# Performance work log

Measured on AMD Instinct MI355X. Metric: run time of the kernel, lower is better.

## Reference

```python
import jax, jax.numpy as jnp
import numpy as np

H = 64      # LSTM hidden units
OUT = 10    # dense softmax classes


def setup_inputs() -> dict:
    key = jax.random.key(0)
    k0, k1, k2, k3 = jax.random.split(key, 4)
    B, T, D = 256, 1024, 128
    x = jax.random.normal(k0, (B, T, D), dtype=jnp.float32)
    # small weight scale keeps relu cell state stable over 1024 steps
    W = jax.random.normal(k1, (D, 4 * H), dtype=jnp.float32) * 0.05
    U = jax.random.normal(k2, (H, 4 * H), dtype=jnp.float32) * 0.05
    b = jnp.zeros((4 * H,), jnp.float32)
    Wd = jax.random.normal(k3, (H, OUT), dtype=jnp.float32) * 0.05
    bd = jnp.zeros((OUT,), jnp.float32)
    return {"x": x, "W": W, "U": U, "b": b, "Wd": Wd, "bd": bd}


def hard_sigmoid(z):
    # legacy Keras recurrent_activation default
    return jnp.clip(0.2 * z + 0.5, 0.0, 1.0)


def lstm_last_hidden(x, W, U, b):
    # x: [B,T,D] -> last hidden state [B,H]
    B = x.shape[0]
    xw = jnp.einsum('btd,dg->btg', x, W) + b  # [B,T,4H] input projection, computed once

    def step(carry, xt):
        h, c = carry
        z = xt + h @ U  # [B,4H]
        i = hard_sigmoid(z[:, :H])
        f = hard_sigmoid(z[:, H:2 * H])
        g = jax.nn.relu(z[:, 2 * H:3 * H])   # activation='relu' (candidate)
        o = hard_sigmoid(z[:, 3 * H:])
        c = f * c + i * g
        h = o * jax.nn.relu(c)               # activation='relu' on cell output
        return (h, c), None

    h0 = jnp.zeros((B, H), x.dtype)
    (h, _), _ = jax.lax.scan(step, (h0, h0), jnp.swapaxes(xw, 0, 1))
    return h


def reference(x, W, U, b, Wd, bd):
    h = lstm_last_hidden(x, W, U, b)          # [B,H]
    return jax.nn.softmax(h @ Wd + bd, axis=-1)  # [B,OUT]
```

## Files before the change

kernel.cpp:

```cpp
#include <hip/hip_runtime.h>
#include <hip/hip_bf16.h>

#define Hh   64
#define G4   256
#define Dd   128
#define Bsz  256
#define Tt   1024
#define NOUT 10

typedef __bf16  bf16x8 __attribute__((ext_vector_type(8)));
typedef float   f32x4v __attribute__((ext_vector_type(4)));


__global__ __launch_bounds__(128)
void k0_wt(const float* __restrict__ W, __bf16* __restrict__ Wt) {
    const int n = blockIdx.x;
    const int k = threadIdx.x;
    Wt[(size_t)n * Dd + k] = (__bf16)W[(size_t)k * G4 + n];
}

#define K1_RT 8

__global__ __launch_bounds__(256)
void k1_mfma(const float* __restrict__ x, const __bf16* __restrict__ Wt,
             const float* __restrict__ bias, __bf16* __restrict__ xw) {
    const int tid = threadIdx.x;
    const int w   = tid >> 6;
    const int l   = tid & 63;
    const int r16 = l & 15;
    const int kq  = l >> 4;
    const size_t rowbase = (size_t)blockIdx.x * (16 * K1_RT);

    bf16x8 bfr[4][4];
    float  bval[4];
#pragma unroll
    for (int ct = 0; ct < 4; ++ct) {
        const int col = w * 64 + ct * 16 + r16;
        const __bf16* wp = Wt + (size_t)col * Dd + kq * 8;
#pragma unroll
        for (int kk = 0; kk < 4; ++kk)
            bfr[ct][kk] = *(const bf16x8*)(wp + kk * 32);
        bval[ct] = bias[col];
    }

    for (int rt = 0; rt < K1_RT; ++rt) {
        const size_t arow = rowbase + rt * 16 + r16;
        const float* xr = x + arow * Dd + kq * 8;
        bf16x8 afr[4];
#pragma unroll
        for (int kk = 0; kk < 4; ++kk) {
            const float4 lo = *(const float4*)(xr + kk * 32);
            const float4 hi = *(const float4*)(xr + kk * 32 + 4);
            afr[kk][0] = (__bf16)lo.x; afr[kk][1] = (__bf16)lo.y;
            afr[kk][2] = (__bf16)lo.z; afr[kk][3] = (__bf16)lo.w;
            afr[kk][4] = (__bf16)hi.x; afr[kk][5] = (__bf16)hi.y;
            afr[kk][6] = (__bf16)hi.z; afr[kk][7] = (__bf16)hi.w;
        }
        f32x4v acc[4];
#pragma unroll
        for (int ct = 0; ct < 4; ++ct)
            acc[ct] = (f32x4v){bval[ct], bval[ct], bval[ct], bval[ct]};
#pragma unroll
        for (int ct = 0; ct < 4; ++ct)
#pragma unroll
            for (int kk = 0; kk < 4; ++kk)
                acc[ct] = __builtin_amdgcn_mfma_f32_16x16x32_bf16(
                              afr[kk], bfr[ct][kk], acc[ct], 0, 0, 0);

        const size_t orow0 = rowbase + rt * 16 + kq * 4;
#pragma unroll
        for (int ct = 0; ct < 4; ++ct) {
            const int pcol = ct * 64 + w * 16 + r16;
#pragma unroll
            for (int r = 0; r < 4; ++r)
                xw[(orow0 + r) * G4 + pcol] = (__bf16)acc[ct][r];
        }
    }
}

__global__ __launch_bounds__(256)
void k2_scan(const __bf16* __restrict__ xw, const float* __restrict__ U,
             float* __restrict__ hout) {
    const int tid = threadIdx.x;
    const int w   = tid >> 6;
    const int l   = tid & 63;
    const int q   = l >> 4;
    const int m   = l & 15;
    const int brow = blockIdx.x;

    __shared__ __align__(16) float hs[2][Hh];

    const int ucol = 64 * q + 16 * w + m;
    float u[Hh];
#pragma unroll
    for (int j = 0; j < Hh; ++j) u[j] = U[(size_t)j * G4 + ucol];

    float c = 0.f;
    if (tid < Hh) { hs[0][tid] = 0.f; }

    const __bf16* __restrict__ xwrow = xw + (size_t)brow * Tt * G4 + tid;
    float zin = (float)xwrow[0];
    __syncthreads();

    for (int t = 0; t < Tt; ++t) {
        const int p  = t & 1;
        const int tn = (t + 1 < Tt) ? (t + 1) : (Tt - 1);
        const float znext = (float)xwrow[(size_t)tn * G4];

        float a0 = zin, a1 = 0.f, a2 = 0.f, a3 = 0.f;
#pragma unroll
        for (int j = 0; j < Hh; j += 4) {
            const f32x4v h4 = *(const f32x4v*)&hs[p][j];
            a0 = fmaf(h4[0], u[j + 0], a0);
            a1 = fmaf(h4[1], u[j + 1], a1);
            a2 = fmaf(h4[2], u[j + 2], a2);
            a3 = fmaf(h4[3], u[j + 3], a3);
        }
        const float z = (a0 + a1) + (a2 + a3);

        const float v0 = z;
        const float v1 = __shfl_xor(z, 16);
        const float v2 = __shfl_xor(z, 32);
        const float v3 = __shfl_xor(v1, 32);
        const float zi = (q == 0) ? v0 : (q == 1) ? v1 : (q == 2) ? v2 : v3;
        const float zf = (q == 1) ? v0 : (q == 0) ? v1 : (q == 3) ? v2 : v3;
        const float zg = (q == 2) ? v0 : (q == 3) ? v1 : (q == 0) ? v2 : v3;
        const float zo = (q == 3) ? v0 : (q == 2) ? v1 : (q == 1) ? v2 : v3;

        const float gi = fminf(fmaxf(0.2f * zi + 0.5f, 0.f), 1.f);
        const float gf = fminf(fmaxf(0.2f * zf + 0.5f, 0.f), 1.f);
        const float gg = fmaxf(zg, 0.f);
        const float go = fminf(fmaxf(0.2f * zo + 0.5f, 0.f), 1.f);
        c = gf * c + gi * gg;
        const float h = go * fmaxf(c, 0.f);

        if (q == 0) hs[1 - p][16 * w + m] = h;
        zin = znext;
        __syncthreads();
    }
    if (tid < Hh) hout[(size_t)brow * Hh + tid] = hs[0][tid];
}

__global__ __launch_bounds__(256)
void k3_dense(const float* __restrict__ hin, const float* __restrict__ Wd,
              const float* __restrict__ bd, float* __restrict__ out) {
    __shared__ float wd[Hh * NOUT];
    __shared__ float bds[NOUT];
    for (int i = threadIdx.x; i < Hh * NOUT; i += blockDim.x) wd[i] = Wd[i];
    if (threadIdx.x < NOUT) bds[threadIdx.x] = bd[threadIdx.x];
    __syncthreads();

    const int r = threadIdx.x;
    if (r < Bsz) {
        float hrow[Hh];
#pragma unroll
        for (int j = 0; j < Hh; ++j) hrow[j] = hin[(size_t)r * Hh + j];
        float logits[NOUT];
#pragma unroll
        for (int o = 0; o < NOUT; ++o) {
            float acc = bds[o];
#pragma unroll
            for (int j = 0; j < Hh; ++j) acc = fmaf(hrow[j], wd[j * NOUT + o], acc);
            logits[o] = acc;
        }
        float mx = logits[0];
#pragma unroll
        for (int o = 1; o < NOUT; ++o) mx = fmaxf(mx, logits[o]);
        float s = 0.f;
#pragma unroll
        for (int o = 0; o < NOUT; ++o) { logits[o] = expf(logits[o] - mx); s += logits[o]; }
        const float inv = 1.f / s;
#pragma unroll
        for (int o = 0; o < NOUT; ++o) out[(size_t)r * NOUT + o] = logits[o] * inv;
    }
}

extern "C" void kernel_launch(void* const* d_in, const int* in_sizes, int n_in,
                              void* d_out, int out_size, void* d_ws, size_t ws_size,
                              hipStream_t stream) {
    const float* x  = (const float*)d_in[0];
    const float* W  = (const float*)d_in[1];
    const float* U  = (const float*)d_in[2];
    const float* b  = (const float*)d_in[3];
    const float* Wd = (const float*)d_in[4];
    const float* bd = (const float*)d_in[5];
    float* out = (float*)d_out;

    const size_t xw_bytes = (size_t)Bsz * Tt * G4 * sizeof(__bf16);
    __bf16* xw   = (__bf16*)d_ws;
    float*  hbuf = (float*)((char*)d_ws + xw_bytes);
    __bf16* Wt   = (__bf16*)((char*)d_ws + xw_bytes + (size_t)Bsz * Hh * sizeof(float));

    k0_wt<<<G4, Dd, 0, stream>>>(W, Wt);
    k1_mfma<<<(Bsz * Tt) / (16 * K1_RT), 256, 0, stream>>>(x, Wt, b, xw);
    k2_scan<<<Bsz, 256, 0, stream>>>(xw, U, hbuf);
    k3_dense<<<1, 256, 0, stream>>>(hbuf, Wd, bd, out);
}
```

Before: 619.0 us.

## Batch 16 sequences per block in LSTM scan using bf16 MFMA recurrence

```diff
diff --git a/kernel.cpp b/kernel.cpp
--- a/kernel.cpp
+++ b/kernel.cpp
@@ -9,8 +9,8 @@
 #define NOUT 10
 
 typedef __bf16  bf16x8 __attribute__((ext_vector_type(8)));
+typedef __bf16  bf16x4 __attribute__((ext_vector_type(4)));
 typedef float   f32x4v __attribute__((ext_vector_type(4)));
-
 
 __global__ __launch_bounds__(128)
 void k0_wt(const float* __restrict__ W, __bf16* __restrict__ Wt) {
@@ -70,10 +70,10 @@
         const size_t orow0 = rowbase + rt * 16 + kq * 4;
 #pragma unroll
         for (int ct = 0; ct < 4; ++ct) {
-            const int pcol = ct * 64 + w * 16 + r16;
-#pragma unroll
-            for (int r = 0; r < 4; ++r)
-                xw[(orow0 + r) * G4 + pcol] = (__bf16)acc[ct][r];
+            const int col = w * 64 + ct * 16 + r16;
+#pragma unroll
+            for (int rr = 0; rr < 4; ++rr)
+                xw[(orow0 + rr) * G4 + col] = (__bf16)acc[ct][rr];
         }
     }
 }
@@ -86,59 +86,99 @@
     const int l   = tid & 63;
     const int q   = l >> 4;
     const int m   = l & 15;
-    const int brow = blockIdx.x;
-
-    __shared__ __align__(16) float hs[2][Hh];
-
-    const int ucol = 64 * q + 16 * w + m;
-    float u[Hh];
-#pragma unroll
-    for (int j = 0; j < Hh; ++j) u[j] = U[(size_t)j * G4 + ucol];
-
-    float c = 0.f;
-    if (tid < Hh) { hs[0][tid] = 0.f; }
-
-    const __bf16* __restrict__ xwrow = xw + (size_t)brow * Tt * G4 + tid;
-    float zin = (float)xwrow[0];
-    __syncthreads();
-
-    for (int t = 0; t < Tt; ++t) {
-        const int p  = t & 1;
-        const int tn = (t + 1 < Tt) ? (t + 1) : (Tt - 1);
-        const float znext = (float)xwrow[(size_t)tn * G4];
-
-        float a0 = zin, a1 = 0.f, a2 = 0.f, a3 = 0.f;
-#pragma unroll
-        for (int j = 0; j < Hh; j += 4) {
-            const f32x4v h4 = *(const f32x4v*)&hs[p][j];
-            a0 = fmaf(h4[0], u[j + 0], a0);
-            a1 = fmaf(h4[1], u[j + 1], a1);
-            a2 = fmaf(h4[2], u[j + 2], a2);
-            a3 = fmaf(h4[3], u[j + 3], a3);
-        }
-        const float z = (a0 + a1) + (a2 + a3);
-
-        const float v0 = z;
-        const float v1 = __shfl_xor(z, 16);
-        const float v2 = __shfl_xor(z, 32);
-        const float v3 = __shfl_xor(v1, 32);
-        const float zi = (q == 0) ? v0 : (q == 1) ? v1 : (q == 2) ? v2 : v3;
-        const float zf = (q == 1) ? v0 : (q == 0) ? v1 : (q == 3) ? v2 : v3;
-        const float zg = (q == 2) ? v0 : (q == 3) ? v1 : (q == 0) ? v2 : v3;
-        const float zo = (q == 3) ? v0 : (q == 2) ? v1 : (q == 1) ? v2 : v3;
-
-        const float gi = fminf(fmaxf(0.2f * zi + 0.5f, 0.f), 1.f);
-        const float gf = fminf(fmaxf(0.2f * zf + 0.5f, 0.f), 1.f);
-        const float gg = fmaxf(zg, 0.f);
-        const float go = fminf(fmaxf(0.2f * zo + 0.5f, 0.f), 1.f);
-        c = gf * c + gi * gg;
-        const float h = go * fmaxf(c, 0.f);
-
-        if (q == 0) hs[1 - p][16 * w + m] = h;
-        zin = znext;
-        __syncthreads();
-    }
-    if (tid < Hh) hout[(size_t)brow * Hh + tid] = hs[0][tid];
+    const int b0  = blockIdx.x * 16;
+
+    __shared__ __align__(16) unsigned char hlds[2][16 * 128];
+
+    bf16x8 au[4][2];
+#pragma unroll
+    for (int tt = 0; tt < 4; ++tt)
+#pragma unroll
+        for (int s = 0; s < 2; ++s)
+#pragma unroll
+            for (int j = 0; j < 8; ++j)
+                au[tt][s][j] = (__bf16)U[(size_t)(q * 8 + j + 32 * s) * G4
+                                         + 16 * (w + 4 * tt) + m];
+
+    const unsigned char* lanebase = (const unsigned char*)xw
+        + (size_t)(b0 + m) * Tt * (G4 * 2) + (size_t)(16 * w + 4 * q) * 2;
+
+    uint2 xzp[4][4];
+#pragma unroll
+    for (int s4 = 0; s4 < 4; ++s4)
+#pragma unroll
+        for (int tt = 0; tt < 4; ++tt)
+            xzp[s4][tt] = *(const uint2*)(lanebase + (size_t)s4 * 512 + tt * 128);
+
+    bf16x8 bh0{}, bh1{};
+    float  c[4]  = {0.f, 0.f, 0.f, 0.f};
+    float  hcur[4] = {0.f, 0.f, 0.f, 0.f};
+
+    const int wslot = ((2 * w + (q >> 1)) ^ (m & 7));
+    const int wbyte = m * 128 + (wslot << 4) + ((q & 1) << 3);
+    const int rbyte0 = m * 128 + (((q + 0) ^ (m & 7)) << 4);
+    const int rbyte1 = m * 128 + (((q + 4) ^ (m & 7)) << 4);
+
+    for (int t0 = 0; t0 < Tt; t0 += 4) {
+#pragma unroll
+        for (int s4 = 0; s4 < 4; ++s4) {
+            const int t = t0 + s4;
+            const int p = t & 1;
+
+            f32x4v acc[4];
+#pragma unroll
+            for (int tt = 0; tt < 4; ++tt) {
+                const uint2 pr = xzp[s4][tt];
+                acc[tt][0] = __builtin_bit_cast(float, pr.x << 16);
+                acc[tt][1] = __builtin_bit_cast(float, pr.x & 0xFFFF0000u);
+                acc[tt][2] = __builtin_bit_cast(float, pr.y << 16);
+                acc[tt][3] = __builtin_bit_cast(float, pr.y & 0xFFFF0000u);
+            }
+
+            {
+                int tp = t + 4; if (tp > Tt - 1) tp = Tt - 1;
+                const unsigned char* pb = lanebase + (size_t)tp * 512;
+#pragma unroll
+                for (int tt = 0; tt < 4; ++tt)
+                    xzp[s4][tt] = *(const uint2*)(pb + tt * 128);
+            }
+
+#pragma unroll
+            for (int tt = 0; tt < 4; ++tt) {
+                acc[tt] = __builtin_amdgcn_mfma_f32_16x16x32_bf16(
+                              au[tt][0], bh0, acc[tt], 0, 0, 0);
+                acc[tt] = __builtin_amdgcn_mfma_f32_16x16x32_bf16(
+                              au[tt][1], bh1, acc[tt], 0, 0, 0);
+            }
+
+            bf16x4 hv;
+#pragma unroll
+            for (int r = 0; r < 4; ++r) {
+                const float zi = acc[0][r], zf = acc[1][r];
+                const float zg = acc[2][r], zo = acc[3][r];
+                const float gi = fminf(fmaxf(fmaf(0.2f, zi, 0.5f), 0.f), 1.f);
+                const float gf = fminf(fmaxf(fmaf(0.2f, zf, 0.5f), 0.f), 1.f);
+                const float gg = fmaxf(zg, 0.f);
+                const float go = fminf(fmaxf(fmaf(0.2f, zo, 0.5f), 0.f), 1.f);
+                c[r] = fmaf(gf, c[r], gi * gg);
+                const float h = go * fmaxf(c[r], 0.f);
+                hcur[r] = h;
+                hv[r] = (__bf16)h;
+            }
+
+            *(bf16x4*)&hlds[p ^ 1][wbyte] = hv;
+            asm volatile("s_waitcnt lgkmcnt(0)" ::: "memory");
+            __builtin_amdgcn_sched_barrier(0);
+            __builtin_amdgcn_s_barrier();
+            __builtin_amdgcn_sched_barrier(0);
+
+            bh0 = *(const bf16x8*)&hlds[p ^ 1][rbyte0];
+            bh1 = *(const bf16x8*)&hlds[p ^ 1][rbyte1];
+        }
+    }
+
+    *(float4*)&hout[(size_t)(b0 + m) * Hh + 16 * w + 4 * q] =
+        (float4){hcur[0], hcur[1], hcur[2], hcur[3]};
 }
 
 __global__ __launch_bounds__(256)
@@ -193,6 +233,6 @@
 
     k0_wt<<<G4, Dd, 0, stream>>>(W, Wt);
     k1_mfma<<<(Bsz * Tt) / (16 * K1_RT), 256, 0, stream>>>(x, Wt, b, xw);
-    k2_scan<<<Bsz, 256, 0, stream>>>(xw, U, hbuf);
+    k2_scan<<<Bsz / 16, 256, 0, stream>>>(xw, U, hbuf);
     k3_dense<<<1, 256, 0, stream>>>(hbuf, Wd, bd, out);
 }
```

Result: faster. 570.8 us (-7.8%).
